# Optimization experiments

Hardware: AMD Instinct MI355X
Metric: run time of the kernel (lower is better)

## Reference

```python
import jax, jax.numpy as jnp
import numpy as np

N_C, N_M, N_D = 100000, 50000, 10000
E = 800000
F_IN, F_H, F_OUT = 128, 64, 64
EPS = 1e-12


def setup_inputs() -> dict:
    key = jax.random.key(0)
    ks = jax.random.split(key, 24)
    s = 1.0 / np.sqrt(F_IN)
    s2 = 1.0 / np.sqrt(F_H)
    inp = {
        'x_circ': jax.random.normal(ks[0], (N_C, F_IN), jnp.float32),
        'x_mir': jax.random.normal(ks[1], (N_M, F_IN), jnp.float32),
        'x_dis': jax.random.normal(ks[2], (N_D, F_IN), jnp.float32),
        'src_cm': jax.random.randint(ks[3], (E,), 0, N_C, jnp.int32),
        'dst_cm': jax.random.randint(ks[4], (E,), 0, N_M, jnp.int32),
        'src_md': jax.random.randint(ks[5], (E,), 0, N_M, jnp.int32),
        'dst_md': jax.random.randint(ks[6], (E,), 0, N_D, jnp.int32),
        'src_cd': jax.random.randint(ks[7], (E,), 0, N_C, jnp.int32),
        'dst_cd': jax.random.randint(ks[8], (E,), 0, N_D, jnp.int32),
        'src_mc': jax.random.randint(ks[9], (E,), 0, N_M, jnp.int32),
        'dst_mc': jax.random.randint(ks[10], (E,), 0, N_C, jnp.int32),
        'src_dm': jax.random.randint(ks[11], (E,), 0, N_D, jnp.int32),
        'dst_dm': jax.random.randint(ks[12], (E,), 0, N_M, jnp.int32),
        'src_dc': jax.random.randint(ks[13], (E,), 0, N_D, jnp.int32),
        'dst_dc': jax.random.randint(ks[14], (E,), 0, N_C, jnp.int32),
        'W1_l': jax.random.uniform(ks[15], (6, F_IN, F_H), jnp.float32, -s, s),
        'W1_r': jax.random.uniform(ks[16], (6, F_IN, F_H), jnp.float32, -s, s),
        'b1': jnp.zeros((6, F_H), jnp.float32),
        'W2_l': jax.random.uniform(ks[17], (6, F_H, F_OUT), jnp.float32, -s2, s2),
        'W2_r': jax.random.uniform(ks[18], (6, F_H, F_OUT), jnp.float32, -s2, s2),
        'b2': jnp.zeros((6, F_OUT), jnp.float32),
        'W_res': jax.random.uniform(ks[19], (3, F_IN, F_OUT), jnp.float32, -s, s),
        'b_res': jnp.zeros((3, F_OUT), jnp.float32),
    }
    return inp


def _sage(x_src, x_dst, src, dst, Wl, bl, Wr, n_dst):
    # PyG SAGEConv (mean aggr): lin_l(mean_{j in N(i)} x_j) + lin_r(x_i)
    msg = x_src[src]                                              # [E, F] gather
    agg = jax.ops.segment_sum(msg, dst, num_segments=n_dst)      # [n_dst, F]
    cnt = jax.ops.segment_sum(jnp.ones_like(dst, dtype=x_src.dtype), dst,
                              num_segments=n_dst)
    mean = agg / jnp.maximum(cnt, 1.0)[:, None]
    return mean @ Wl + bl + x_dst @ Wr


def _hetero_layer(xc, xm, xd, Wl, Wr, b, edges):
    # relation order: 0=c->m, 1=m->d, 2=c->d, 3=m->c, 4=d->m, 5=d->c
    h_m = 0.5 * (_sage(xc, xm, edges['cm'][0], edges['cm'][1], Wl[0], b[0], Wr[0], xm.shape[0])
                 + _sage(xd, xm, edges['dm'][0], edges['dm'][1], Wl[4], b[4], Wr[4], xm.shape[0]))
    h_d = 0.5 * (_sage(xm, xd, edges['md'][0], edges['md'][1], Wl[1], b[1], Wr[1], xd.shape[0])
                 + _sage(xc, xd, edges['cd'][0], edges['cd'][1], Wl[2], b[2], Wr[2], xd.shape[0]))
    h_c = 0.5 * (_sage(xm, xc, edges['mc'][0], edges['mc'][1], Wl[3], b[3], Wr[3], xc.shape[0])
                 + _sage(xd, xc, edges['dc'][0], edges['dc'][1], Wl[5], b[5], Wr[5], xc.shape[0]))
    return h_c, h_m, h_d


def _l2norm(x):
    n = jnp.sqrt(jnp.sum(x * x, axis=1, keepdims=True))
    return x / jnp.maximum(n, EPS)


def reference(x_circ, x_mir, x_dis,
              src_cm, dst_cm, src_md, dst_md, src_cd, dst_cd,
              src_mc, dst_mc, src_dm, dst_dm, src_dc, dst_dc,
              W1_l, W1_r, b1, W2_l, W2_r, b2, W_res, b_res):
    edges = {'cm': (src_cm, dst_cm), 'md': (src_md, dst_md), 'cd': (src_cd, dst_cd),
             'mc': (src_mc, dst_mc), 'dm': (src_dm, dst_dm), 'dc': (src_dc, dst_dc)}
    h_c, h_m, h_d = _hetero_layer(x_circ, x_mir, x_dis, W1_l, W1_r, b1, edges)
    h_c, h_m, h_d = jax.nn.relu(h_c), jax.nn.relu(h_m), jax.nn.relu(h_d)  # dropout = identity (eval)
    o_c, o_m, o_d = _hetero_layer(h_c, h_m, h_d, W2_l, W2_r, b2, edges)
    o_c = o_c + x_circ @ W_res[0] + b_res[0]
    o_m = o_m + x_mir @ W_res[1] + b_res[1]
    o_d = o_d + x_dis @ W_res[2] + b_res[2]
    return _l2norm(o_c), _l2norm(o_m), _l2norm(o_d)
```

## Files before the change

kernel.cpp:

```cpp
#include <hip/hip_runtime.h>
#include <cstdint>
#include <cstddef>

#define EE        800000
#define NC        100000
#define NM        50000
#define ND        10000
#define NSLOTS    320000

#define SB0 0
#define SB1 50000
#define SB2 60000
#define SB3 70000
#define SB4 170000
#define SB5 220000

#define R0 0
#define R1 100000
#define R2 150000
#define R3 250000
#define R4 300000
#define R5 310000

#define NB 2400
#define EPB 4096
#define EBL 196
#define PPB 4096
#define PBL 196
#define BCAP 4096

typedef _Float16 f16x8 __attribute__((ext_vector_type(8)));
typedef float f32x4 __attribute__((ext_vector_type(4)));
typedef float f32x2 __attribute__((ext_vector_type(2)));

__device__ __forceinline__ void bucket_split(int rel, int d, int& lb, int& dl) {
    switch (rel) {
        case 0: case 4: lb = d / 125; dl = d - lb * 125; break;
        case 1: case 2: lb = d / 25;  dl = d - lb * 25;  break;
        default:        lb = d / 250; dl = d - lb * 250; break;
    }
}

__device__ __forceinline__ unsigned f2bf(float f) {
    unsigned b = __float_as_uint(f);
    return (b + 0x7FFFu + ((b >> 16) & 1u)) >> 16;
}

__global__ __launch_bounds__(256) void cvt_hist_k(
    const float* __restrict__ W1l, const float* __restrict__ W2l,
    const float* __restrict__ W1r, const float* __restrict__ W2r,
    const float* __restrict__ Wres, const float* __restrict__ b1,
    const float* __restrict__ b2, const float* __restrict__ bres,
    _Float16* __restrict__ Wt1, _Float16* __restrict__ Wt2,
    _Float16* __restrict__ Wz1t, _Float16* __restrict__ Wz2t,
    _Float16* __restrict__ Wrest, float* __restrict__ bz1, float* __restrict__ bz2,
    int* __restrict__ bhist,
    const int* __restrict__ d0, const int* __restrict__ d1, const int* __restrict__ d2,
    const int* __restrict__ d3, const int* __restrict__ d4, const int* __restrict__ d5)
{
    __shared__ int hl[400];
    int blk = blockIdx.x;
    int tid = threadIdx.x;
    if (blk < 192) {
        const int raT[3] = {0, 1, 3}, rbT[3] = {4, 2, 5}, rmT[3] = {1, 2, 0};
        int i = blk * 256 + tid;
        if (i < 6 * 128 * 64) {
            int r = i >> 13, rem = i & 8191, k = rem >> 6, n = rem & 63;
            Wt1[(size_t)r * 8192 + (size_t)n * 128 + k] = (_Float16)W1l[i];
        }
        if (i < 6 * 64 * 64) {
            int r = i >> 12, rem = i & 4095, k = rem >> 6, n = rem & 63;
            Wt2[(size_t)r * 4096 + (size_t)n * 64 + k] = (_Float16)W2l[i];
        }
        if (i < 3 * 8192) {
            int t = i >> 13, rem = i & 8191, n = rem >> 7, k = rem & 127;
            float v = 0.5f * (W1r[(size_t)raT[t] * 8192 + k * 64 + n] +
                              W1r[(size_t)rbT[t] * 8192 + k * 64 + n]);
            Wz1t[i] = (_Float16)v;
        }
        if (i < 3 * 4096) {
            int t = i >> 12, rem = i & 4095, n = rem >> 6, k = rem & 63;
            float v = 0.5f * (W2r[(size_t)raT[t] * 4096 + k * 64 + n] +
                              W2r[(size_t)rbT[t] * 4096 + k * 64 + n]);
            Wz2t[i] = (_Float16)v;
        }
        if (i < 3 * 8192) {
            int t = i >> 13, rem = i & 8191, n = rem >> 7, k = rem & 127;
            Wrest[i] = (_Float16)Wres[(size_t)rmT[t] * 8192 + k * 64 + n];
        }
        if (i < 192) {
            int t = i >> 6, n = i & 63;
            bz1[i] = 0.5f * (b1[raT[t] * 64 + n] + b1[rbT[t] * 64 + n]);
            bz2[i] = 0.5f * (b2[raT[t] * 64 + n] + b2[rbT[t] * 64 + n]) + bres[rmT[t] * 64 + n];
        }
        return;
    }
    int hb = blk - 192;
    int rel = hb / EBL;
    int chunk = hb - rel * EBL;
    const int* dst;
    switch (rel) {
        case 0: dst = d0; break; case 1: dst = d1; break; case 2: dst = d2; break;
        case 3: dst = d3; break; case 4: dst = d4; break; default: dst = d5; break;
    }
    for (int i = tid; i < 400; i += 256) hl[i] = 0;
    __syncthreads();
    int e0 = chunk * EPB;
#pragma unroll
    for (int t = 0; t < EPB / 256; ++t) {
        int e = e0 + t * 256 + tid;
        if (e < EE) {
            int lb, dl;
            bucket_split(rel, dst[e], lb, dl);
            atomicAdd(&hl[lb], 1);
        }
    }
    __syncthreads();
    for (int i = tid; i < 400; i += 256) {
        int v = hl[i];
        if (v) atomicAdd(&bhist[rel * 400 + i], v);
    }
}

__global__ __launch_bounds__(256) void bucket_scan_k(const int* __restrict__ bhist,
    int* __restrict__ bOff, int* __restrict__ bCur, int* __restrict__ off)
{
    __shared__ int lds[256];
    int tid = threadIdx.x;
    int v[10];
    int tot = 0;
#pragma unroll
    for (int t = 0; t < 10; ++t) {
        int idx = tid * 10 + t;
        int x = (idx < NB) ? bhist[idx] : 0;
        v[t] = tot;
        tot += x;
    }
    lds[tid] = tot;
    __syncthreads();
    for (int o = 1; o < 256; o <<= 1) {
        int x = 0;
        if (tid >= o) x = lds[tid - o];
        __syncthreads();
        lds[tid] += x;
        __syncthreads();
    }
    int excl = lds[tid] - tot;
#pragma unroll
    for (int t = 0; t < 10; ++t) {
        int idx = tid * 10 + t;
        if (idx < NB) {
            int val = excl + v[t];
            bOff[idx] = val;
            bCur[idx] = val;
        }
    }
    if (tid == 255) {
        bOff[NB] = lds[255];
        off[NSLOTS] = lds[255];
    }
}

__global__ __launch_bounds__(256) void part_fused1_k(
    const int* __restrict__ s0, const int* __restrict__ d0,
    const int* __restrict__ s1, const int* __restrict__ d1,
    const int* __restrict__ s2, const int* __restrict__ d2,
    const int* __restrict__ s3, const int* __restrict__ d3,
    const int* __restrict__ s4, const int* __restrict__ d4,
    const int* __restrict__ s5, const int* __restrict__ d5,
    int* __restrict__ bCur, int* __restrict__ bArr,
    const float* __restrict__ fc, const float* __restrict__ fm, const float* __restrict__ fd,
    const _Float16* __restrict__ Wt1, const _Float16* __restrict__ Wz1t,
    const float* __restrict__ bz1,
    unsigned short* __restrict__ y,
    float* __restrict__ hc, float* __restrict__ hm, float* __restrict__ hd)
{
    __shared__ __align__(16) char smem[29376];
    int blk = blockIdx.x;
    int tid = threadIdx.x;
    if (blk < 6 * PBL) {
        int* hist = (int*)smem;
        int* scan_ = hist + 400;
        int* gb = scan_ + 400;
        int* sorted = gb + 400;
        unsigned short* lbs16 = (unsigned short*)(sorted + PPB);
        int rel = blk / PBL;
        int chunk = blk - rel * PBL;
        const int* src; const int* dst;
        switch (rel) {
            case 0: src = s0; dst = d0; break;
            case 1: src = s1; dst = d1; break;
            case 2: src = s2; dst = d2; break;
            case 3: src = s3; dst = d3; break;
            case 4: src = s4; dst = d4; break;
            default: src = s5; dst = d5; break;
        }
        for (int i = tid; i < 400; i += 256) hist[i] = 0;
        __syncthreads();
        int e0 = chunk * PPB;
        int e1 = e0 + PPB; if (e1 > EE) e1 = EE;
        int m = e1 - e0;
        for (int i = tid; i < m; i += 256) {
            int lb, dl;
            bucket_split(rel, dst[e0 + i], lb, dl);
            atomicAdd(&hist[lb], 1);
        }
        __syncthreads();
        if (tid < 64) {
            int carry = 0;
#pragma unroll
            for (int c = 0; c < 7; ++c) {
                int idx = c * 64 + tid;
                int orig = (idx < 400) ? hist[idx] : 0;
                int v = orig;
#pragma unroll
                for (int o = 1; o < 64; o <<= 1) {
                    int u = __shfl_up(v, o);
                    if (tid >= o) v += u;
                }
                if (idx < 400) scan_[idx] = carry + v - orig;
                carry += __shfl(v, 63);
            }
        }
        for (int i = tid; i < 400; i += 256) {
            int c = hist[i];
            gb[i] = c ? atomicAdd(&bCur[rel * 400 + i], c) : 0;
        }
        __syncthreads();
        for (int i = tid; i < 400; i += 256) hist[i] = 0;
        __syncthreads();
        for (int i = tid; i < m; i += 256) {
            int d = dst[e0 + i];
            int s = src[e0 + i];
            int lb, dl;
            bucket_split(rel, d, lb, dl);
            int r = atomicAdd(&hist[lb], 1);
            int pos = scan_[lb] + r;
            sorted[pos] = (dl << 17) | s;
            lbs16[pos] = (unsigned short)lb;
        }
        __syncthreads();
        for (int i = tid; i < m; i += 256) {
            int lb = lbs16[i];
            bArr[gb[lb] + i - scan_[lb]] = sorted[i];
        }
        return;
    }
    _Float16* xs = (_Float16*)smem;
    int b = blk - 6 * PBL;
    int t, lb;
    if (b < 782)      { t = 0; lb = b; }
    else if (b < 939) { t = 1; lb = b - 782; }
    else              { t = 2; lb = b - 939; }
    const float* x; int n; float* zo; int ra, rb, roA, roB;
    switch (t) {
        case 0: x = fm; n = NM; zo = hm; ra = 1; rb = 3; roA = R1; roB = R3; break;
        case 1: x = fd; n = ND; zo = hd; ra = 4; rb = 5; roA = R4; roB = R5; break;
        default: x = fc; n = NC; zo = hc; ra = 0; rb = 2; roA = R0; roB = R2; break;
    }
    int node0 = lb * 64;
    for (int idx = tid; idx < 64 * 16; idx += 256) {
        int nn = idx >> 4, c8 = idx & 15;
        int g = node0 + nn;
        float4 u0 = make_float4(0.f, 0.f, 0.f, 0.f), u1 = u0;
        if (g < n) {
            const float4* p = (const float4*)(x + (size_t)g * 128 + c8 * 8);
            u0 = p[0]; u1 = p[1];
        }
        f16x8 v;
        v[0] = (_Float16)u0.x; v[1] = (_Float16)u0.y; v[2] = (_Float16)u0.z; v[3] = (_Float16)u0.w;
        v[4] = (_Float16)u1.x; v[5] = (_Float16)u1.y; v[6] = (_Float16)u1.z; v[7] = (_Float16)u1.w;
        *(f16x8*)(xs + nn * 136 + c8 * 8) = v;
    }
    __syncthreads();
    int lane = tid & 63, wv = tid >> 6;
    int lr = lane & 15, lg = lane >> 4;
    if (wv < 2) {
        int rel = wv ? rb : ra;
        int ro  = wv ? roB : roA;
        const _Float16* W = Wt1 + (size_t)rel * 8192;
        unsigned short* yo = y + (size_t)ro * 64;
        f16x8 bf[4][4];
#pragma unroll
        for (int kt = 0; kt < 4; ++kt)
#pragma unroll
            for (int nt = 0; nt < 4; ++nt)
                bf[kt][nt] = *(const f16x8*)(W + (size_t)(nt * 16 + lr) * 128 + kt * 32 + lg * 8);
#pragma unroll
        for (int rt = 0; rt < 4; ++rt) {
            f32x4 acc[4];
#pragma unroll
            for (int nt = 0; nt < 4; ++nt) { acc[nt][0] = 0.f; acc[nt][1] = 0.f; acc[nt][2] = 0.f; acc[nt][3] = 0.f; }
            const _Float16* xrow = xs + (rt * 16 + lr) * 136;
#pragma unroll
            for (int kt = 0; kt < 4; ++kt) {
                f16x8 af = *(const f16x8*)(xrow + kt * 32 + lg * 8);
#pragma unroll
                for (int nt = 0; nt < 4; ++nt)
                    acc[nt] = __builtin_amdgcn_mfma_f32_16x16x32_f16(af, bf[kt][nt], acc[nt], 0, 0, 0);
            }
            int orow = node0 + rt * 16 + lg * 4;
#pragma unroll
            for (int rg = 0; rg < 4; ++rg) {
                int gg = orow + rg;
                if (gg < n) {
                    unsigned short* yr = yo + (size_t)gg * 64 + lr;
#pragma unroll
                    for (int nt = 0; nt < 4; ++nt)
                        yr[nt * 16] = (unsigned short)f2bf(acc[nt][rg]);
                }
            }
        }
    } else {
        const _Float16* W = Wz1t + (size_t)t * 8192;
        const float* bz = bz1 + t * 64;
        f16x8 bf[4][4];
#pragma unroll
        for (int kt = 0; kt < 4; ++kt)
#pragma unroll
            for (int nt = 0; nt < 4; ++nt)
                bf[kt][nt] = *(const f16x8*)(W + (size_t)(nt * 16 + lr) * 128 + kt * 32 + lg * 8);
        int rbase = (wv - 2) * 32;
#pragma unroll
        for (int rt = 0; rt < 2; ++rt) {
            f32x4 acc[4];
#pragma unroll
            for (int nt = 0; nt < 4; ++nt) {
                float bv = bz[nt * 16 + lr];
                acc[nt][0] = bv; acc[nt][1] = bv; acc[nt][2] = bv; acc[nt][3] = bv;
            }
            const _Float16* xrow = xs + (rbase + rt * 16 + lr) * 136;
#pragma unroll
            for (int kt = 0; kt < 4; ++kt) {
                f16x8 af = *(const f16x8*)(xrow + kt * 32 + lg * 8);
#pragma unroll
                for (int nt = 0; nt < 4; ++nt)
                    acc[nt] = __builtin_amdgcn_mfma_f32_16x16x32_f16(af, bf[kt][nt], acc[nt], 0, 0, 0);
            }
            int orow = node0 + rbase + rt * 16 + lg * 4;
#pragma unroll
            for (int rg = 0; rg < 4; ++rg) {
                int gg = orow + rg;
                if (gg < n) {
                    float* zr = zo + (size_t)gg * 64 + lr;
#pragma unroll
                    for (int nt = 0; nt < 4; ++nt)
                        zr[nt * 16] = acc[nt][rg];
                }
            }
        }
    }
}

__global__ __launch_bounds__(256) void bucket_build_k(
    const int* __restrict__ bArr, const int* __restrict__ bOff,
    int* __restrict__ off, int* __restrict__ csr)
{
    __shared__ int cnt[256];
    __shared__ int sc[256];
    __shared__ int cur[256];
    __shared__ int stage[BCAP];
    int b = blockIdx.x;
    int tid = threadIdx.x;
    int r = b / 400;
    int lb = b - r * 400;
    int spb, sbase;
    switch (r) {
        case 0: spb = 125; sbase = SB0; break;
        case 1: spb = 25;  sbase = SB1; break;
        case 2: spb = 25;  sbase = SB2; break;
        case 3: spb = 250; sbase = SB3; break;
        case 4: spb = 125; sbase = SB4; break;
        default: spb = 250; sbase = SB5; break;
    }
    int slot0 = lb * spb;
    int e0 = bOff[b], e1 = bOff[b + 1];
    int m = e1 - e0;
    int ms = m < BCAP ? m : BCAP;

    cnt[tid] = 0;
    __syncthreads();
    for (int i = tid; i < ms; i += 256) {
        int p = bArr[e0 + i];
        stage[i] = p;
        atomicAdd(&cnt[p >> 17], 1);
    }
    __syncthreads();
    int x = cnt[tid];
    sc[tid] = x;
    __syncthreads();
    for (int o = 1; o < 256; o <<= 1) {
        int y = 0;
        if (tid >= o) y = sc[tid - o];
        __syncthreads();
        sc[tid] += y;
        __syncthreads();
    }
    int excl = sc[tid] - x;
    cur[tid] = excl;
    if (tid < spb) off[sbase + slot0 + tid] = e0 + excl;
    __syncthreads();
    for (int i = tid; i < ms; i += 256) {
        int p = stage[i];
        int pos = atomicAdd(&cur[p >> 17], 1);
        csr[e0 + pos] = (p & 0x1FFFF) << 7;
    }
}

__global__ __launch_bounds__(256) void fused2_k(
    const float* __restrict__ hc, const float* __restrict__ hm, const float* __restrict__ hd,
    const float* __restrict__ xc, const float* __restrict__ xm, const float* __restrict__ xd,
    const _Float16* __restrict__ Wt2, const _Float16* __restrict__ Wz2t,
    const _Float16* __restrict__ Wrest, const float* __restrict__ bz2,
    unsigned short* __restrict__ y,
    float* __restrict__ oc, float* __restrict__ om, float* __restrict__ od)
{
    int b = blockIdx.x;
    int t, lb;
    if (b < 782)      { t = 0; lb = b; }
    else if (b < 939) { t = 1; lb = b - 782; }
    else              { t = 2; lb = b - 939; }
    const float *h, *x; int n; float* zo; int ra, rb, roA, roB;
    switch (t) {
        case 0: h = hm; x = xm; n = NM; zo = om; ra = 1; rb = 3; roA = R1; roB = R3; break;
        case 1: h = hd; x = xd; n = ND; zo = od; ra = 4; rb = 5; roA = R4; roB = R5; break;
        default: h = hc; x = xc; n = NC; zo = oc; ra = 0; rb = 2; roA = R0; roB = R2; break;
    }
    __shared__ _Float16 hs[64 * 72];
    __shared__ _Float16 xs[64 * 136];
    int tid = threadIdx.x;
    int node0 = lb * 64;
    for (int idx = tid; idx < 64 * 8; idx += 256) {
        int nn = idx >> 3, c8 = idx & 7;
        int g = node0 + nn;
        float4 u0 = make_float4(0.f, 0.f, 0.f, 0.f), u1 = u0;
        if (g < n) {
            const float4* p = (const float4*)(h + (size_t)g * 64 + c8 * 8);
            u0 = p[0]; u1 = p[1];
        }
        f16x8 v;
        v[0] = (_Float16)u0.x; v[1] = (_Float16)u0.y; v[2] = (_Float16)u0.z; v[3] = (_Float16)u0.w;
        v[4] = (_Float16)u1.x; v[5] = (_Float16)u1.y; v[6] = (_Float16)u1.z; v[7] = (_Float16)u1.w;
        *(f16x8*)(hs + nn * 72 + c8 * 8) = v;
    }
    for (int idx = tid; idx < 64 * 16; idx += 256) {
        int nn = idx >> 4, c8 = idx & 15;
        int g = node0 + nn;
        float4 u0 = make_float4(0.f, 0.f, 0.f, 0.f), u1 = u0;
        if (g < n) {
            const float4* p = (const float4*)(x + (size_t)g * 128 + c8 * 8);
            u0 = p[0]; u1 = p[1];
        }
        f16x8 v;
        v[0] = (_Float16)u0.x; v[1] = (_Float16)u0.y; v[2] = (_Float16)u0.z; v[3] = (_Float16)u0.w;
        v[4] = (_Float16)u1.x; v[5] = (_Float16)u1.y; v[6] = (_Float16)u1.z; v[7] = (_Float16)u1.w;
        *(f16x8*)(xs + nn * 136 + c8 * 8) = v;
    }
    __syncthreads();
    int lane = tid & 63, wv = tid >> 6;
    int lr = lane & 15, lg = lane >> 4;
    if (wv < 2) {
        int rel = wv ? rb : ra;
        int ro  = wv ? roB : roA;
        const _Float16* W = Wt2 + (size_t)rel * 4096;
        unsigned short* yo = y + (size_t)ro * 64;
        f16x8 bf[2][4];
#pragma unroll
        for (int kt = 0; kt < 2; ++kt)
#pragma unroll
            for (int nt = 0; nt < 4; ++nt)
                bf[kt][nt] = *(const f16x8*)(W + (size_t)(nt * 16 + lr) * 64 + kt * 32 + lg * 8);
#pragma unroll
        for (int rt = 0; rt < 4; ++rt) {
            f32x4 acc[4];
#pragma unroll
            for (int nt = 0; nt < 4; ++nt) { acc[nt][0] = 0.f; acc[nt][1] = 0.f; acc[nt][2] = 0.f; acc[nt][3] = 0.f; }
            const _Float16* hrow = hs + (rt * 16 + lr) * 72;
#pragma unroll
            for (int kt = 0; kt < 2; ++kt) {
                f16x8 af = *(const f16x8*)(hrow + kt * 32 + lg * 8);
#pragma unroll
                for (int nt = 0; nt < 4; ++nt)
                    acc[nt] = __builtin_amdgcn_mfma_f32_16x16x32_f16(af, bf[kt][nt], acc[nt], 0, 0, 0);
            }
            int orow = node0 + rt * 16 + lg * 4;
#pragma unroll
            for (int rg = 0; rg < 4; ++rg) {
                int gg = orow + rg;
                if (gg < n) {
                    unsigned short* yr = yo + (size_t)gg * 64 + lr;
#pragma unroll
                    for (int nt = 0; nt < 4; ++nt)
                        yr[nt * 16] = (unsigned short)f2bf(acc[nt][rg]);
                }
            }
        }
    } else {
        const _Float16* Wh = Wz2t + (size_t)t * 4096;
        const _Float16* Wx = Wrest + (size_t)t * 8192;
        const float* bz = bz2 + t * 64;
        f16x8 bfh[2][4];
#pragma unroll
        for (int kt = 0; kt < 2; ++kt)
#pragma unroll
            for (int nt = 0; nt < 4; ++nt)
                bfh[kt][nt] = *(const f16x8*)(Wh + (size_t)(nt * 16 + lr) * 64 + kt * 32 + lg * 8);
        f16x8 bfx[4][4];
#pragma unroll
        for (int kt = 0; kt < 4; ++kt)
#pragma unroll
            for (int nt = 0; nt < 4; ++nt)
                bfx[kt][nt] = *(const f16x8*)(Wx + (size_t)(nt * 16 + lr) * 128 + kt * 32 + lg * 8);
        int rbase = (wv - 2) * 32;
#pragma unroll
        for (int rt = 0; rt < 2; ++rt) {
            f32x4 acc[4];
#pragma unroll
            for (int nt = 0; nt < 4; ++nt) {
                float bv = bz[nt * 16 + lr];
                acc[nt][0] = bv; acc[nt][1] = bv; acc[nt][2] = bv; acc[nt][3] = bv;
            }
            const _Float16* hrow = hs + (rbase + rt * 16 + lr) * 72;
            const _Float16* xrow = xs + (rbase + rt * 16 + lr) * 136;
#pragma unroll
            for (int kt = 0; kt < 2; ++kt) {
                f16x8 af = *(const f16x8*)(hrow + kt * 32 + lg * 8);
#pragma unroll
                for (int nt = 0; nt < 4; ++nt)
                    acc[nt] = __builtin_amdgcn_mfma_f32_16x16x32_f16(af, bfh[kt][nt], acc[nt], 0, 0, 0);
            }
#pragma unroll
            for (int kt = 0; kt < 4; ++kt) {
                f16x8 af = *(const f16x8*)(xrow + kt * 32 + lg * 8);
#pragma unroll
                for (int nt = 0; nt < 4; ++nt)
                    acc[nt] = __builtin_amdgcn_mfma_f32_16x16x32_f16(af, bfx[kt][nt], acc[nt], 0, 0, 0);
            }
            int orow = node0 + rbase + rt * 16 + lg * 4;
#pragma unroll
            for (int rg = 0; rg < 4; ++rg) {
                int gg = orow + rg;
                if (gg < n) {
                    float* zr = zo + (size_t)gg * 64 + lr;
#pragma unroll
                    for (int nt = 0; nt < 4; ++nt)
                        zr[nt * 16] = acc[nt][rg];
                }
            }
        }
    }
}

__device__ __forceinline__ void acc_pk(f32x2* a, uint4 v) {
    f32x2 t0, t1, t2, t3;
    t0[0] = __uint_as_float(v.x << 16); t0[1] = __uint_as_float(v.x & 0xFFFF0000u);
    t1[0] = __uint_as_float(v.y << 16); t1[1] = __uint_as_float(v.y & 0xFFFF0000u);
    t2[0] = __uint_as_float(v.z << 16); t2[1] = __uint_as_float(v.z & 0xFFFF0000u);
    t3[0] = __uint_as_float(v.w << 16); t3[1] = __uint_as_float(v.w & 0xFFFF0000u);
    a[0] += t0; a[1] += t1; a[2] += t2; a[3] += t3;
}

template<bool RELU, bool NORM>
__global__ __launch_bounds__(256) void agg_all_k(
    const unsigned short* __restrict__ y, const int* __restrict__ off,
    const int* __restrict__ csr,
    float* __restrict__ ioc, float* __restrict__ iom, float* __restrict__ iod)
{
    int w = blockIdx.x * 4 + (threadIdx.x >> 6);
    int t, wid;
    if (w < NM) { t = 0; wid = w; }
    else if (w < NM + ND) { t = 1; wid = w - NM; }
    else { t = 2; wid = w - NM - ND; }
    const int *o1, *o2; const unsigned short *y1, *y2; float* io;
    switch (t) {
        case 0: o1 = off + SB0; o2 = off + SB4; y1 = y + (size_t)R0 * 64; y2 = y + (size_t)R4 * 64; io = iom; break;
        case 1: o1 = off + SB1; o2 = off + SB2; y1 = y + (size_t)R1 * 64; y2 = y + (size_t)R2 * 64; io = iod; break;
        default: o1 = off + SB3; o2 = off + SB5; y1 = y + (size_t)R3 * 64; y2 = y + (size_t)R5 * 64; io = ioc; break;
    }
    int lane = threadIdx.x & 63;
    int g = lane >> 3, ql = lane & 7;
    int qoff = ql * 16;
    f32x2 acc[4];
#pragma unroll
    for (int j = 0; j < 4; ++j) { acc[j][0] = 0.f; acc[j][1] = 0.f; }
    {
        const char* yb = (const char*)y1 + qoff;
        int e0 = o1[wid], e1 = o1[wid + 1];
        f32x2 a[4];
#pragma unroll
        for (int j = 0; j < 4; ++j) { a[j][0] = 0.f; a[j][1] = 0.f; }
        int e = e0 + g;
        int i0 = 0, i1 = 0;
        if (e < e1) i0 = csr[e];
        if (e + 8 < e1) i1 = csr[e + 8];
        for (; e + 8 < e1; e += 16) {
            int p0 = csr[e + 16];
            int p1 = csr[e + 24];
            uint4 vA = *(const uint4*)(yb + (unsigned)i0);
            uint4 vB = *(const uint4*)(yb + (unsigned)i1);
            acc_pk(a, vA);
            acc_pk(a, vB);
            i0 = p0; i1 = p1;
        }
        if (e < e1) {
            uint4 v = *(const uint4*)(yb + (unsigned)i0);
            acc_pk(a, v);
        }
        float inv = 1.f / fmaxf((float)(e1 - e0), 1.f);
        f32x2 iv; iv[0] = inv; iv[1] = inv;
#pragma unroll
        for (int j = 0; j < 4; ++j) acc[j] += a[j] * iv;
    }
    {
        const char* yb = (const char*)y2 + qoff;
        int e0 = o2[wid], e1 = o2[wid + 1];
        f32x2 a[4];
#pragma unroll
        for (int j = 0; j < 4; ++j) { a[j][0] = 0.f; a[j][1] = 0.f; }
        int e = e0 + g;
        int i0 = 0, i1 = 0;
        if (e < e1) i0 = csr[e];
        if (e + 8 < e1) i1 = csr[e + 8];
        for (; e + 8 < e1; e += 16) {
            int p0 = csr[e + 16];
            int p1 = csr[e + 24];
            uint4 vA = *(const uint4*)(yb + (unsigned)i0);
            uint4 vB = *(const uint4*)(yb + (unsigned)i1);
            acc_pk(a, vA);
            acc_pk(a, vB);
            i0 = p0; i1 = p1;
        }
        if (e < e1) {
            uint4 v = *(const uint4*)(yb + (unsigned)i0);
            acc_pk(a, v);
        }
        float inv = 1.f / fmaxf((float)(e1 - e0), 1.f);
        f32x2 iv; iv[0] = inv; iv[1] = inv;
#pragma unroll
        for (int j = 0; j < 4; ++j) acc[j] += a[j] * iv;
    }
#pragma unroll
    for (int j = 0; j < 4; ++j) {
#pragma unroll
        for (int c = 0; c < 2; ++c) {
            float v = acc[j][c];
            v += __shfl_xor(v, 8);
            v += __shfl_xor(v, 16);
            v += __shfl_xor(v, 32);
            acc[j][c] = v;
        }
    }
    if (g == 0) {
        float* iorow = io + ((size_t)wid << 6) + ql * 8;
        float4 z1 = *((const float4*)iorow);
        float4 z2 = *((const float4*)(iorow + 4));
        float o[8];
        o[0] = 0.5f * acc[0][0] + z1.x; o[1] = 0.5f * acc[0][1] + z1.y;
        o[2] = 0.5f * acc[1][0] + z1.z; o[3] = 0.5f * acc[1][1] + z1.w;
        o[4] = 0.5f * acc[2][0] + z2.x; o[5] = 0.5f * acc[2][1] + z2.y;
        o[6] = 0.5f * acc[3][0] + z2.z; o[7] = 0.5f * acc[3][1] + z2.w;
        if (RELU) {
#pragma unroll
            for (int j = 0; j < 8; ++j) o[j] = fmaxf(o[j], 0.f);
        }
        if (NORM) {
            float ss = 0.f;
#pragma unroll
            for (int j = 0; j < 8; ++j) ss += o[j] * o[j];
            ss += __shfl_xor(ss, 1); ss += __shfl_xor(ss, 2); ss += __shfl_xor(ss, 4);
            float r = 1.f / fmaxf(sqrtf(ss), 1e-12f);
#pragma unroll
            for (int j = 0; j < 8; ++j) o[j] *= r;
        }
        *((float4*)iorow) = make_float4(o[0], o[1], o[2], o[3]);
        *((float4*)(iorow + 4)) = make_float4(o[4], o[5], o[6], o[7]);
    }
}

extern "C" void kernel_launch(void* const* d_in, const int* in_sizes, int n_in,
                              void* d_out, int out_size, void* d_ws, size_t ws_size,
                              hipStream_t stream) {
    const float* x_c = (const float*)d_in[0];
    const float* x_m = (const float*)d_in[1];
    const float* x_d = (const float*)d_in[2];
    const int* src_cm = (const int*)d_in[3];
    const int* dst_cm = (const int*)d_in[4];
    const int* src_md = (const int*)d_in[5];
    const int* dst_md = (const int*)d_in[6];
    const int* src_cd = (const int*)d_in[7];
    const int* dst_cd = (const int*)d_in[8];
    const int* src_mc = (const int*)d_in[9];
    const int* dst_mc = (const int*)d_in[10];
    const int* src_dm = (const int*)d_in[11];
    const int* dst_dm = (const int*)d_in[12];
    const int* src_dc = (const int*)d_in[13];
    const int* dst_dc = (const int*)d_in[14];
    const float* W1l = (const float*)d_in[15];
    const float* W1r = (const float*)d_in[16];
    const float* b1 = (const float*)d_in[17];
    const float* W2l = (const float*)d_in[18];
    const float* W2r = (const float*)d_in[19];
    const float* b2 = (const float*)d_in[20];
    const float* Wres = (const float*)d_in[21];
    const float* bres = (const float*)d_in[22];
    float* out = (float*)d_out;

    int* off = (int*)d_ws;
    int* csr = off + 320064;
    int* bArr = csr;
    int* bhist = csr + 4800000;
    int* bOff = bhist + 2400;
    int* bCur = bOff + 2404;
    float* h = (float*)(bCur + 2404);
    float* h_c = h;
    float* h_m = h_c + (size_t)NC * 64;
    float* h_d = h_m + (size_t)NM * 64;
    unsigned short* y = (unsigned short*)(h + (size_t)160000 * 64);
    _Float16* Wt1 = (_Float16*)(y + (size_t)320000 * 64);
    _Float16* Wt2 = Wt1 + 6 * 64 * 128;
    _Float16* Wz1t = Wt2 + 6 * 64 * 64;
    _Float16* Wz2t = Wz1t + 3 * 64 * 128;
    _Float16* Wrest = Wz2t + 3 * 64 * 64;
    float* bz1 = (float*)(Wrest + 3 * 64 * 128);
    float* bz2 = bz1 + 192;

    float* out_c = out;
    float* out_m = out + (size_t)NC * 64;
    float* out_d = out_m + (size_t)NM * 64;

    hipMemsetAsync(bhist, 0, NB * sizeof(int), stream);

    cvt_hist_k<<<192 + EBL * 6, 256, 0, stream>>>(
        W1l, W2l, W1r, W2r, Wres, b1, b2, bres,
        Wt1, Wt2, Wz1t, Wz2t, Wrest, bz1, bz2, bhist,
        dst_cm, dst_md, dst_cd, dst_mc, dst_dm, dst_dc);

    bucket_scan_k<<<1, 256, 0, stream>>>(bhist, bOff, bCur, off);

    part_fused1_k<<<6 * PBL + 2502, 256, 0, stream>>>(
        src_cm, dst_cm, src_md, dst_md, src_cd, dst_cd,
        src_mc, dst_mc, src_dm, dst_dm, src_dc, dst_dc,
        bCur, bArr,
        x_c, x_m, x_d, Wt1, Wz1t, bz1, y, h_c, h_m, h_d);

    bucket_build_k<<<NB, 256, 0, stream>>>(bArr, bOff, off, csr);

    agg_all_k<true, false><<<40000, 256, 0, stream>>>(y, off, csr, h_c, h_m, h_d);

    fused2_k<<<2502, 256, 0, stream>>>(h_c, h_m, h_d, x_c, x_m, x_d,
                                       Wt2, Wz2t, Wrest, bz2, y, out_c, out_m, out_d);

    agg_all_k<false, true><<<40000, 256, 0, stream>>>(y, off, csr, out_c, out_m, out_d);
}
```

Measured before the change: 580.2 us.

## Split partition into its own kernel and fuse bucket build with layer-1 GEMM

The edge partition work moves into a standalone 512-thread kernel. The CSR bucket-build blocks now share a launch with the layer-1 node GEMM blocks instead of with the partition. The GEMM work therefore overlaps the bucket build rather than the partition, the launch count stays the same, and partition blocks get more threads per block. LDS per block in the fused kernel shrinks, which may raise occupancy. The risk is that build blocks become the critical path, or that the partition kernel loses the GEMM overlap it had before.

```diff
diff --git a/kernel.cpp b/kernel.cpp
--- a/kernel.cpp
+++ b/kernel.cpp
@@ -161,93 +161,149 @@
     }
 }
 
-__global__ __launch_bounds__(256) void part_fused1_k(
+__global__ __launch_bounds__(512) void partition_k(
     const int* __restrict__ s0, const int* __restrict__ d0,
     const int* __restrict__ s1, const int* __restrict__ d1,
     const int* __restrict__ s2, const int* __restrict__ d2,
     const int* __restrict__ s3, const int* __restrict__ d3,
     const int* __restrict__ s4, const int* __restrict__ d4,
     const int* __restrict__ s5, const int* __restrict__ d5,
-    int* __restrict__ bCur, int* __restrict__ bArr,
+    int* __restrict__ bCur, int* __restrict__ bArr)
+{
+    __shared__ int hist[400];
+    __shared__ int scan_[400];
+    __shared__ int gb[400];
+    __shared__ int sorted[PPB];
+    __shared__ unsigned short lbs16[PPB];
+    int blk = blockIdx.x;
+    int tid = threadIdx.x;
+    int rel = blk / PBL;
+    int chunk = blk - rel * PBL;
+    const int* src; const int* dst;
+    switch (rel) {
+        case 0: src = s0; dst = d0; break;
+        case 1: src = s1; dst = d1; break;
+        case 2: src = s2; dst = d2; break;
+        case 3: src = s3; dst = d3; break;
+        case 4: src = s4; dst = d4; break;
+        default: src = s5; dst = d5; break;
+    }
+    for (int i = tid; i < 400; i += 512) hist[i] = 0;
+    __syncthreads();
+    int e0 = chunk * PPB;
+    int e1 = e0 + PPB; if (e1 > EE) e1 = EE;
+    int m = e1 - e0;
+    for (int i = tid; i < m; i += 512) {
+        int lb, dl;
+        bucket_split(rel, dst[e0 + i], lb, dl);
+        atomicAdd(&hist[lb], 1);
+    }
+    __syncthreads();
+    if (tid < 64) {
+        int carry = 0;
+#pragma unroll
+        for (int c = 0; c < 7; ++c) {
+            int idx = c * 64 + tid;
+            int orig = (idx < 400) ? hist[idx] : 0;
+            int v = orig;
+#pragma unroll
+            for (int o = 1; o < 64; o <<= 1) {
+                int u = __shfl_up(v, o);
+                if (tid >= o) v += u;
+            }
+            if (idx < 400) scan_[idx] = carry + v - orig;
+            carry += __shfl(v, 63);
+        }
+    }
+    for (int i = tid; i < 400; i += 512) {
+        int c = hist[i];
+        gb[i] = c ? atomicAdd(&bCur[rel * 400 + i], c) : 0;
+    }
+    __syncthreads();
+    for (int i = tid; i < 400; i += 512) hist[i] = 0;
+    __syncthreads();
+    for (int i = tid; i < m; i += 512) {
+        int d = dst[e0 + i];
+        int s = src[e0 + i];
+        int lb, dl;
+        bucket_split(rel, d, lb, dl);
+        int r = atomicAdd(&hist[lb], 1);
+        int pos = scan_[lb] + r;
+        sorted[pos] = (dl << 17) | s;
+        lbs16[pos] = (unsigned short)lb;
+    }
+    __syncthreads();
+    for (int i = tid; i < m; i += 512) {
+        int lb = lbs16[i];
+        bArr[gb[lb] + i - scan_[lb]] = sorted[i];
+    }
+}
+
+__global__ __launch_bounds__(256) void build_fused1_k(
+    const int* __restrict__ bArr, const int* __restrict__ bOff,
+    int* __restrict__ off, int* __restrict__ csr,
     const float* __restrict__ fc, const float* __restrict__ fm, const float* __restrict__ fd,
     const _Float16* __restrict__ Wt1, const _Float16* __restrict__ Wz1t,
     const float* __restrict__ bz1,
     unsigned short* __restrict__ y,
     float* __restrict__ hc, float* __restrict__ hm, float* __restrict__ hd)
 {
-    __shared__ __align__(16) char smem[29376];
+    __shared__ __align__(16) char smem[19456];
     int blk = blockIdx.x;
     int tid = threadIdx.x;
-    if (blk < 6 * PBL) {
-        int* hist = (int*)smem;
-        int* scan_ = hist + 400;
-        int* gb = scan_ + 400;
-        int* sorted = gb + 400;
-        unsigned short* lbs16 = (unsigned short*)(sorted + PPB);
-        int rel = blk / PBL;
-        int chunk = blk - rel * PBL;
-        const int* src; const int* dst;
-        switch (rel) {
-            case 0: src = s0; dst = d0; break;
-            case 1: src = s1; dst = d1; break;
-            case 2: src = s2; dst = d2; break;
-            case 3: src = s3; dst = d3; break;
-            case 4: src = s4; dst = d4; break;
-            default: src = s5; dst = d5; break;
-        }
-        for (int i = tid; i < 400; i += 256) hist[i] = 0;
+    if (blk < NB) {
+        int* cnt = (int*)smem;
+        int* sc = cnt + 256;
+        int* cur = sc + 256;
+        int* stage = cur + 256;
+        int b = blk;
+        int r = b / 400;
+        int lb = b - r * 400;
+        int spb, sbase;
+        switch (r) {
+            case 0: spb = 125; sbase = SB0; break;
+            case 1: spb = 25;  sbase = SB1; break;
+            case 2: spb = 25;  sbase = SB2; break;
+            case 3: spb = 250; sbase = SB3; break;
+            case 4: spb = 125; sbase = SB4; break;
+            default: spb = 250; sbase = SB5; break;
+        }
+        int slot0 = lb * spb;
+        int e0 = bOff[b], e1 = bOff[b + 1];
+        int m = e1 - e0;
+        int ms = m < BCAP ? m : BCAP;
+
+        cnt[tid] = 0;
         __syncthreads();
-        int e0 = chunk * PPB;
-        int e1 = e0 + PPB; if (e1 > EE) e1 = EE;
-        int m = e1 - e0;
-        for (int i = tid; i < m; i += 256) {
-            int lb, dl;
-            bucket_split(rel, dst[e0 + i], lb, dl);
-            atomicAdd(&hist[lb], 1);
+        for (int i = tid; i < ms; i += 256) {
+            int p = bArr[e0 + i];
+            stage[i] = p;
+            atomicAdd(&cnt[p >> 17], 1);
         }
         __syncthreads();
-        if (tid < 64) {
-            int carry = 0;
-#pragma unroll
-            for (int c = 0; c < 7; ++c) {
-                int idx = c * 64 + tid;
-                int orig = (idx < 400) ? hist[idx] : 0;
-                int v = orig;
-#pragma unroll
-                for (int o = 1; o < 64; o <<= 1) {
-                    int u = __shfl_up(v, o);
-                    if (tid >= o) v += u;
-                }
-                if (idx < 400) scan_[idx] = carry + v - orig;
-                carry += __shfl(v, 63);
-            }
-        }
-        for (int i = tid; i < 400; i += 256) {
-            int c = hist[i];
-            gb[i] = c ? atomicAdd(&bCur[rel * 400 + i], c) : 0;
-        }
+        int x = cnt[tid];
+        sc[tid] = x;
         __syncthreads();
-        for (int i = tid; i < 400; i += 256) hist[i] = 0;
+        for (int o = 1; o < 256; o <<= 1) {
+            int yv = 0;
+            if (tid >= o) yv = sc[tid - o];
+            __syncthreads();
+            sc[tid] += yv;
+            __syncthreads();
+        }
+        int excl = sc[tid] - x;
+        cur[tid] = excl;
+        if (tid < spb) off[sbase + slot0 + tid] = e0 + excl;
         __syncthreads();
-        for (int i = tid; i < m; i += 256) {
-            int d = dst[e0 + i];
-            int s = src[e0 + i];
-            int lb, dl;
-            bucket_split(rel, d, lb, dl);
-            int r = atomicAdd(&hist[lb], 1);
-            int pos = scan_[lb] + r;
-            sorted[pos] = (dl << 17) | s;
-            lbs16[pos] = (unsigned short)lb;
-        }
-        __syncthreads();
-        for (int i = tid; i < m; i += 256) {
-            int lb = lbs16[i];
-            bArr[gb[lb] + i - scan_[lb]] = sorted[i];
+        for (int i = tid; i < ms; i += 256) {
+            int p = stage[i];
+            int pos = atomicAdd(&cur[p >> 17], 1);
+            csr[e0 + pos] = (p & 0x1FFFF) << 7;
         }
         return;
     }
     _Float16* xs = (_Float16*)smem;
-    int b = blk - 6 * PBL;
+    int b = blk - NB;
     int t, lb;
     if (b < 782)      { t = 0; lb = b; }
     else if (b < 939) { t = 1; lb = b - 782; }
@@ -349,61 +405,6 @@
                 }
             }
         }
-    }
-}
-
-__global__ __launch_bounds__(256) void bucket_build_k(
-    const int* __restrict__ bArr, const int* __restrict__ bOff,
-    int* __restrict__ off, int* __restrict__ csr)
-{
-    __shared__ int cnt[256];
-    __shared__ int sc[256];
-    __shared__ int cur[256];
-    __shared__ int stage[BCAP];
-    int b = blockIdx.x;
-    int tid = threadIdx.x;
-    int r = b / 400;
-    int lb = b - r * 400;
-    int spb, sbase;
-    switch (r) {
-        case 0: spb = 125; sbase = SB0; break;
-        case 1: spb = 25;  sbase = SB1; break;
-        case 2: spb = 25;  sbase = SB2; break;
-        case 3: spb = 250; sbase = SB3; break;
-        case 4: spb = 125; sbase = SB4; break;
-        default: spb = 250; sbase = SB5; break;
-    }
-    int slot0 = lb * spb;
-    int e0 = bOff[b], e1 = bOff[b + 1];
-    int m = e1 - e0;
-    int ms = m < BCAP ? m : BCAP;
-
-    cnt[tid] = 0;
-    __syncthreads();
-    for (int i = tid; i < ms; i += 256) {
-        int p = bArr[e0 + i];
-        stage[i] = p;
-        atomicAdd(&cnt[p >> 17], 1);
-    }
-    __syncthreads();
-    int x = cnt[tid];
-    sc[tid] = x;
-    __syncthreads();
-    for (int o = 1; o < 256; o <<= 1) {
-        int y = 0;
-        if (tid >= o) y = sc[tid - o];
-        __syncthreads();
-        sc[tid] += y;
-        __syncthreads();
-    }
-    int excl = sc[tid] - x;
-    cur[tid] = excl;
-    if (tid < spb) off[sbase + slot0 + tid] = e0 + excl;
-    __syncthreads();
-    for (int i = tid; i < ms; i += 256) {
-        int p = stage[i];
-        int pos = atomicAdd(&cur[p >> 17], 1);
-        csr[e0 + pos] = (p & 0x1FFFF) << 7;
     }
 }
 
@@ -737,13 +738,14 @@
 
     bucket_scan_k<<<1, 256, 0, stream>>>(bhist, bOff, bCur, off);
 
-    part_fused1_k<<<6 * PBL + 2502, 256, 0, stream>>>(
+    partition_k<<<6 * PBL, 512, 0, stream>>>(
         src_cm, dst_cm, src_md, dst_md, src_cd, dst_cd,
         src_mc, dst_mc, src_dm, dst_dm, src_dc, dst_dc,
-        bCur, bArr,
+        bCur, bArr);
+
+    build_fused1_k<<<NB + 2502, 256, 0, stream>>>(
+        bArr, bOff, off, csr,
         x_c, x_m, x_d, Wt1, Wz1t, bz1, y, h_c, h_m, h_d);
-
-    bucket_build_k<<<NB, 256, 0, stream>>>(bArr, bOff, off, csr);
 
     agg_all_k<true, false><<<40000, 256, 0, stream>>>(y, off, csr, h_c, h_m, h_d);
 
```

New measurement: 577.7 us. No clear change (-0.4%).
